# Kernel tuning notes

Measured on AMD Instinct MI355X. Metric: run time of the kernel, lower is better.

Reference implementation:

```python
import jax, jax.numpy as jnp
import numpy as np

# Genome structure (from init_kwargs): ids 0..N_INPUTS-1 are input nodes,
# ids N_NODES-N_OUTPUTS..N_NODES-1 are output nodes.
N_NODES = 32
N_INPUTS = 8
N_OUTPUTS = 4
N_EDGES = 128
BATCH = 524288


def setup_inputs() -> dict:
    key = jax.random.key(0)
    k1, k2, k3, k4 = jax.random.split(key, 4)
    x = jax.random.normal(k1, (N_INPUTS, BATCH), dtype=jnp.float32)
    w = jax.random.normal(k2, (N_EDGES,), dtype=jnp.float32) * 0.5
    src = jax.random.randint(k3, (N_EDGES,), 0, N_NODES, dtype=jnp.int32)
    dst = jax.random.randint(k4, (N_EDGES,), 0, N_NODES, dtype=jnp.int32)
    return {"x": x, "w": w, "src": src, "dst": dst}


def _forward(x, w, src, dst):
    # vals[n] is the [BATCH]-vector state of node n (torch dict-of-scalars, batched).
    vals = jnp.zeros((N_NODES, BATCH), dtype=x.dtype).at[:N_INPUTS].set(x)

    # Faithful to torch: edges are applied SEQUENTIALLY within a sweep
    # (later edges see earlier updates), so use scan, not a parallel scatter.
    def edge_step(v, edge):
        i, o, wv = edge
        return v.at[o].add(jnp.tanh(v[i] * wv)), None

    def iter_body(v, _):
        v, _ = jax.lax.scan(edge_step, v, (src, dst, w))
        return v, None

    # torch: `for _ in range(len(self.g.nodes))` -> N_NODES relaxation sweeps
    vals, _ = jax.lax.scan(iter_body, vals, None, length=N_NODES)

    # torch: stack([tanh(vals[o]) for o in outputs]) -> [N_OUTPUTS, BATCH]
    return jnp.tanh(vals[N_NODES - N_OUTPUTS:])


def reference(x, w, src, dst):
    return _forward(x, w, src, dst)
```

## Files before the change

### kernel.cpp

```cpp
#include <hip/hip_runtime.h>


#define N_NODES   32
#define N_INPUTS  8
#define N_OUTPUTS 4
#define N_EDGES   128
#define BATCH     524288
#define BLOCK     128
#define EPT       2
#define TILE      (BLOCK * EPT)

#define TWO_LOG2E 2.88539008177792681472f

typedef float f32x2 __attribute__((ext_vector_type(2)));

__global__ void EvolvedNet_prep(const float* __restrict__ w,
                                const int*   __restrict__ src,
                                const int*   __restrict__ dst,
                                int* __restrict__ soff, int* __restrict__ doff,
                                float* __restrict__ wk) {
    const int e = threadIdx.x;
    if (e < N_EDGES) {
        soff[e] = src[e] * BLOCK;
        doff[e] = dst[e] * BLOCK;
        wk[e]   = w[e] * TWO_LOG2E;
    }
}

__global__ __launch_bounds__(BLOCK)
void EvolvedNet_80032420593868_kernel(const float* __restrict__ x,
                                      const int*   __restrict__ soff,
                                      const int*   __restrict__ doff,
                                      const float* __restrict__ wk,
                                      float*       __restrict__ out) {
    __shared__ f32x2 vals[N_NODES * BLOCK];

    const int tid = threadIdx.x;
    const int b0  = blockIdx.x * TILE + tid * 2;

#pragma unroll
    for (int n = 0; n < N_INPUTS; ++n)
        vals[n * BLOCK + tid] = *(const f32x2*)&x[n * BATCH + b0];
#pragma unroll
    for (int n = N_INPUTS; n < N_NODES; ++n)
        vals[n * BLOCK + tid] = (f32x2)(0.0f, 0.0f);


    for (int sweep = 0; sweep < N_NODES; ++sweep) {
#pragma unroll 8
        for (int e = 0; e < N_EDGES; ++e) {
            const int   so = soff[e];
            const int   dd = doff[e];
            const float wv = wk[e];

            const f32x2 v  = vals[so + tid];
            const f32x2 dv = vals[dd + tid];
            const f32x2 a  = v * wv;
            f32x2 u;
            u.x = __builtin_amdgcn_exp2f(a.x);
            u.y = __builtin_amdgcn_exp2f(a.y);
            const f32x2 s1 = 1.0f + u;
            f32x2 r;
            r.x = __builtin_amdgcn_rcpf(s1.x);
            r.y = __builtin_amdgcn_rcpf(s1.y);
            const f32x2 t = 1.0f - 2.0f * r;
            vals[dd + tid] = dv + t;
        }
    }

#pragma unroll
    for (int o = 0; o < N_OUTPUTS; ++o) {
        const f32x2 v = vals[(N_NODES - N_OUTPUTS + o) * BLOCK + tid];
        f32x2 t;
        t.x = 1.0f - 2.0f * __builtin_amdgcn_rcpf(1.0f + __builtin_amdgcn_exp2f(v.x * TWO_LOG2E));
        t.y = 1.0f - 2.0f * __builtin_amdgcn_rcpf(1.0f + __builtin_amdgcn_exp2f(v.y * TWO_LOG2E));
        *(f32x2*)&out[o * BATCH + b0] = t;
    }
}

extern "C" void kernel_launch(void* const* d_in, const int* in_sizes, int n_in,
                              void* d_out, int out_size, void* d_ws, size_t ws_size,
                              hipStream_t stream) {
    const float* x   = (const float*)d_in[0];
    const float* w   = (const float*)d_in[1];
    const int*   src = (const int*)d_in[2];
    const int*   dst = (const int*)d_in[3];
    float*       out = (float*)d_out;

    int*   soff = (int*)d_ws;
    int*   doff = soff + N_EDGES;
    float* wkp  = (float*)(doff + N_EDGES);

    EvolvedNet_prep<<<1, 128, 0, stream>>>(w, src, dst, soff, doff, wkp);

    const int grid = BATCH / TILE;
    EvolvedNet_80032420593868_kernel<<<grid, BLOCK, 0, stream>>>(x, soff, doff, wkp, out);
}
```

Measured before the change: 786.3 us.

## Prefetch LDS node values two edges ahead with hazard-forwarding corrections

The edge loop now loads source and destination node values from LDS two edges ahead, so LDS latency overlaps with the tanh math of earlier edges. Because later edges must see earlier updates, this prefetch can read stale values. A prep kernel builds per-edge flag multipliers that add back the tanh results of the previous one or two edges whenever their destination matches the current source or destination. Edge metadata is also packed into 16-byte records so each edge needs one vector load. The cost is extra FMAs, extra registers and an extra fix-up table load per edge.

```diff
diff --git a/kernel.cpp b/kernel.cpp
--- a/kernel.cpp
+++ b/kernel.cpp
@@ -14,25 +14,38 @@
 
 typedef float f32x2 __attribute__((ext_vector_type(2)));
 
+struct __align__(16) ERec  { int soff, doff; float wk, pad; };
+struct __align__(16) EFix  { float g1, g2, h1, h2; };
+
 __global__ void EvolvedNet_prep(const float* __restrict__ w,
                                 const int*   __restrict__ src,
                                 const int*   __restrict__ dst,
-                                int* __restrict__ soff, int* __restrict__ doff,
-                                float* __restrict__ wk) {
+                                ERec* __restrict__ rec,
+                                EFix* __restrict__ fix) {
     const int e = threadIdx.x;
     if (e < N_EDGES) {
-        soff[e] = src[e] * BLOCK;
-        doff[e] = dst[e] * BLOCK;
-        wk[e]   = w[e] * TWO_LOG2E;
+        ERec r;
+        r.soff = src[e] * BLOCK;
+        r.doff = dst[e] * BLOCK;
+        r.wk   = w[e] * TWO_LOG2E;
+        r.pad  = 0.0f;
+        rec[e] = r;
+        const int em1 = (e + N_EDGES - 1) & (N_EDGES - 1);
+        const int em2 = (e + N_EDGES - 2) & (N_EDGES - 1);
+        EFix f;
+        f.g1 = (src[e] == dst[em1]) ? 1.0f : 0.0f;
+        f.g2 = (src[e] == dst[em2]) ? 1.0f : 0.0f;
+        f.h1 = (dst[e] == dst[em1]) ? 1.0f : 0.0f;
+        f.h2 = (dst[e] == dst[em2]) ? 1.0f : 0.0f;
+        fix[e] = f;
     }
 }
 
 __global__ __launch_bounds__(BLOCK)
 void EvolvedNet_80032420593868_kernel(const float* __restrict__ x,
-                                      const int*   __restrict__ soff,
-                                      const int*   __restrict__ doff,
-                                      const float* __restrict__ wk,
-                                      float*       __restrict__ out) {
+                                      const ERec* __restrict__ rec,
+                                      const EFix* __restrict__ fix,
+                                      float*      __restrict__ out) {
     __shared__ f32x2 vals[N_NODES * BLOCK];
 
     const int tid = threadIdx.x;
@@ -46,25 +59,39 @@
         vals[n * BLOCK + tid] = (f32x2)(0.0f, 0.0f);
 
 
+    f32x2 ps0 = vals[rec[0].soff + tid];
+    f32x2 ps1 = vals[rec[1].soff + tid];
+    f32x2 pd0 = vals[rec[0].doff + tid];
+    f32x2 pd1 = vals[rec[1].doff + tid];
+    f32x2 t1 = (f32x2)(0.0f, 0.0f), t2 = (f32x2)(0.0f, 0.0f);
+
     for (int sweep = 0; sweep < N_NODES; ++sweep) {
 #pragma unroll 8
         for (int e = 0; e < N_EDGES; ++e) {
-            const int   so = soff[e];
-            const int   dd = doff[e];
-            const float wv = wk[e];
+            const int  er = (e + 2) & (N_EDGES - 1);
+            const ERec rn = rec[er];
+            const f32x2 vs = vals[rn.soff + tid];
+            const f32x2 vd = vals[rn.doff + tid];
 
-            const f32x2 v  = vals[so + tid];
-            const f32x2 dv = vals[dd + tid];
-            const f32x2 a  = v * wv;
-            f32x2 u;
-            u.x = __builtin_amdgcn_exp2f(a.x);
-            u.y = __builtin_amdgcn_exp2f(a.y);
-            const f32x2 s1 = 1.0f + u;
-            f32x2 r;
-            r.x = __builtin_amdgcn_rcpf(s1.x);
-            r.y = __builtin_amdgcn_rcpf(s1.y);
-            const f32x2 t = 1.0f - 2.0f * r;
-            vals[dd + tid] = dv + t;
+            const ERec r = rec[e];
+            const EFix f = fix[e];
+            f32x2 v  = ps0 + t2 * f.g2;
+            v        = v   + t1 * f.g1;
+            f32x2 dv = pd0 + t2 * f.h2;
+            dv       = dv  + t1 * f.h1;
+
+            const f32x2 a = v * r.wk;
+            f32x2 t;
+            t.x = __builtin_fmaf(-2.0f,
+                    __builtin_amdgcn_rcpf(1.0f + __builtin_amdgcn_exp2f(a.x)), 1.0f);
+            t.y = __builtin_fmaf(-2.0f,
+                    __builtin_amdgcn_rcpf(1.0f + __builtin_amdgcn_exp2f(a.y)), 1.0f);
+
+            vals[r.doff + tid] = dv + t;
+
+            ps0 = ps1; ps1 = vs;
+            pd0 = pd1; pd1 = vd;
+            t2 = t1;   t1 = t;
         }
     }
 
@@ -72,8 +99,10 @@
     for (int o = 0; o < N_OUTPUTS; ++o) {
         const f32x2 v = vals[(N_NODES - N_OUTPUTS + o) * BLOCK + tid];
         f32x2 t;
-        t.x = 1.0f - 2.0f * __builtin_amdgcn_rcpf(1.0f + __builtin_amdgcn_exp2f(v.x * TWO_LOG2E));
-        t.y = 1.0f - 2.0f * __builtin_amdgcn_rcpf(1.0f + __builtin_amdgcn_exp2f(v.y * TWO_LOG2E));
+        t.x = __builtin_fmaf(-2.0f,
+                __builtin_amdgcn_rcpf(1.0f + __builtin_amdgcn_exp2f(v.x * TWO_LOG2E)), 1.0f);
+        t.y = __builtin_fmaf(-2.0f,
+                __builtin_amdgcn_rcpf(1.0f + __builtin_amdgcn_exp2f(v.y * TWO_LOG2E)), 1.0f);
         *(f32x2*)&out[o * BATCH + b0] = t;
     }
 }
@@ -87,12 +116,11 @@
     const int*   dst = (const int*)d_in[3];
     float*       out = (float*)d_out;
 
-    int*   soff = (int*)d_ws;
-    int*   doff = soff + N_EDGES;
-    float* wkp  = (float*)(doff + N_EDGES);
+    ERec* rec = (ERec*)d_ws;
+    EFix* fixp = (EFix*)((char*)d_ws + N_EDGES * sizeof(ERec));
 
-    EvolvedNet_prep<<<1, 128, 0, stream>>>(w, src, dst, soff, doff, wkp);
+    EvolvedNet_prep<<<1, 128, 0, stream>>>(w, src, dst, rec, fixp);
 
     const int grid = BATCH / TILE;
-    EvolvedNet_80032420593868_kernel<<<grid, BLOCK, 0, stream>>>(x, soff, doff, wkp, out);
+    EvolvedNet_80032420593868_kernel<<<grid, BLOCK, 0, stream>>>(x, rec, fixp, out);
 }
```

Result: slower. 969.7 us (+23.3%).

## Prefetch edge source values two edges ahead with forwarding corrections

Applied to the files above, without the earlier changes.

The source-node LDS read for each edge is now issued two edges early, which breaks the serial load-compute-store dependency of the sequential edge loop. The prep kernel precomputes 0/1 flags marking whether an edge's source equals the destination of the previous one or two edges. The kernel uses those flags to add the missed tanh updates back into the prefetched value. Edge offsets, weights and flags now live in VGPRs and are broadcast with readlane instead of per-edge scalar memory loads. The inner loop is fully unrolled, which enlarges the code and raises register pressure.

```diff
diff --git a/kernel.cpp b/kernel.cpp
--- a/kernel.cpp
+++ b/kernel.cpp
@@ -18,25 +18,45 @@
                                 const int*   __restrict__ src,
                                 const int*   __restrict__ dst,
                                 int* __restrict__ soff, int* __restrict__ doff,
-                                float* __restrict__ wk) {
+                                float* __restrict__ wk,
+                                float* __restrict__ g1, float* __restrict__ g2) {
     const int e = threadIdx.x;
     if (e < N_EDGES) {
         soff[e] = src[e] * BLOCK;
         doff[e] = dst[e] * BLOCK;
         wk[e]   = w[e] * TWO_LOG2E;
+        const int em1 = (e + N_EDGES - 1) & (N_EDGES - 1);
+        const int em2 = (e + N_EDGES - 2) & (N_EDGES - 1);
+        g1[e] = (src[e] == dst[em1]) ? 1.0f : 0.0f;
+        g2[e] = (src[e] == dst[em2]) ? 1.0f : 0.0f;
     }
 }
+
+#define RLI(arr, E) __builtin_amdgcn_readlane(arr[(E) >> 6], (E) & 63)
+#define RLF(arr, E) __uint_as_float((unsigned)__builtin_amdgcn_readlane( \
+                        (int)__float_as_uint(arr[(E) >> 6]), (E) & 63))
 
 __global__ __launch_bounds__(BLOCK)
 void EvolvedNet_80032420593868_kernel(const float* __restrict__ x,
                                       const int*   __restrict__ soff,
                                       const int*   __restrict__ doff,
                                       const float* __restrict__ wk,
+                                      const float* __restrict__ g1,
+                                      const float* __restrict__ g2,
                                       float*       __restrict__ out) {
     __shared__ f32x2 vals[N_NODES * BLOCK];
 
-    const int tid = threadIdx.x;
-    const int b0  = blockIdx.x * TILE + tid * 2;
+    const int tid  = threadIdx.x;
+    const int lane = tid & 63;
+    const int b0   = blockIdx.x * TILE + tid * 2;
+
+    int   rs[2], rd[2];
+    float rw[2], r1[2], r2[2];
+    rs[0] = soff[lane];  rs[1] = soff[lane + 64];
+    rd[0] = doff[lane];  rd[1] = doff[lane + 64];
+    rw[0] = wk[lane];    rw[1] = wk[lane + 64];
+    r1[0] = g1[lane];    r1[1] = g1[lane + 64];
+    r2[0] = g2[lane];    r2[1] = g2[lane + 64];
 
 #pragma unroll
     for (int n = 0; n < N_INPUTS; ++n)
@@ -46,25 +66,39 @@
         vals[n * BLOCK + tid] = (f32x2)(0.0f, 0.0f);
 
 
+    f32x2 ps0 = vals[RLI(rs, 0) + tid];
+    f32x2 ps1 = vals[RLI(rs, 1) + tid];
+    f32x2 t1 = (f32x2)(0.0f, 0.0f), t2 = (f32x2)(0.0f, 0.0f);
+
     for (int sweep = 0; sweep < N_NODES; ++sweep) {
-#pragma unroll 8
+#pragma unroll
         for (int e = 0; e < N_EDGES; ++e) {
-            const int   so = soff[e];
-            const int   dd = doff[e];
-            const float wv = wk[e];
+            const int   son = RLI(rs, (e + 2) & (N_EDGES - 1));
+            const f32x2 vs  = vals[son + tid];
 
-            const f32x2 v  = vals[so + tid];
-            const f32x2 dv = vals[dd + tid];
-            const f32x2 a  = v * wv;
-            f32x2 u;
-            u.x = __builtin_amdgcn_exp2f(a.x);
-            u.y = __builtin_amdgcn_exp2f(a.y);
-            const f32x2 s1 = 1.0f + u;
-            f32x2 r;
-            r.x = __builtin_amdgcn_rcpf(s1.x);
-            r.y = __builtin_amdgcn_rcpf(s1.y);
-            const f32x2 t = 1.0f - 2.0f * r;
-            vals[dd + tid] = dv + t;
+            const int   dof = RLI(rd, e);
+            const f32x2 dv  = vals[dof + tid];
+
+            const float g2s = RLF(r2, e);
+            const float g1s = RLF(r1, e);
+            const float wks = RLF(rw, e);
+            f32x2 v;
+            v.x = __builtin_fmaf(g2s, t2.x, ps0.x);
+            v.y = __builtin_fmaf(g2s, t2.y, ps0.y);
+            v.x = __builtin_fmaf(g1s, t1.x, v.x);
+            v.y = __builtin_fmaf(g1s, t1.y, v.y);
+
+            const f32x2 a = v * wks;
+            f32x2 t;
+            t.x = __builtin_fmaf(-2.0f,
+                    __builtin_amdgcn_rcpf(1.0f + __builtin_amdgcn_exp2f(a.x)), 1.0f);
+            t.y = __builtin_fmaf(-2.0f,
+                    __builtin_amdgcn_rcpf(1.0f + __builtin_amdgcn_exp2f(a.y)), 1.0f);
+
+            vals[dof + tid] = dv + t;
+
+            ps0 = ps1; ps1 = vs;
+            t2 = t1;   t1 = t;
         }
     }
 
@@ -72,8 +106,10 @@
     for (int o = 0; o < N_OUTPUTS; ++o) {
         const f32x2 v = vals[(N_NODES - N_OUTPUTS + o) * BLOCK + tid];
         f32x2 t;
-        t.x = 1.0f - 2.0f * __builtin_amdgcn_rcpf(1.0f + __builtin_amdgcn_exp2f(v.x * TWO_LOG2E));
-        t.y = 1.0f - 2.0f * __builtin_amdgcn_rcpf(1.0f + __builtin_amdgcn_exp2f(v.y * TWO_LOG2E));
+        t.x = __builtin_fmaf(-2.0f,
+                __builtin_amdgcn_rcpf(1.0f + __builtin_amdgcn_exp2f(v.x * TWO_LOG2E)), 1.0f);
+        t.y = __builtin_fmaf(-2.0f,
+                __builtin_amdgcn_rcpf(1.0f + __builtin_amdgcn_exp2f(v.y * TWO_LOG2E)), 1.0f);
         *(f32x2*)&out[o * BATCH + b0] = t;
     }
 }
@@ -90,9 +126,12 @@
     int*   soff = (int*)d_ws;
     int*   doff = soff + N_EDGES;
     float* wkp  = (float*)(doff + N_EDGES);
+    float* g1p  = wkp + N_EDGES;
+    float* g2p  = g1p + N_EDGES;
 
-    EvolvedNet_prep<<<1, 128, 0, stream>>>(w, src, dst, soff, doff, wkp);
+    EvolvedNet_prep<<<1, 128, 0, stream>>>(w, src, dst, soff, doff, wkp, g1p, g2p);
 
     const int grid = BATCH / TILE;
-    EvolvedNet_80032420593868_kernel<<<grid, BLOCK, 0, stream>>>(x, soff, doff, wkp, out);
+    EvolvedNet_80032420593868_kernel<<<grid, BLOCK, 0, stream>>>(
+        x, soff, doff, wkp, g1p, g2p, out);
 }
```

Result: slower. 840.6 us (+6.9%).
